# Performance work log

Hardware: AMD Instinct MI355X
Metric: run time of the kernel (lower is better)

Reference implementation:

```python
import jax, jax.numpy as jnp
import numpy as np
from jax import lax

B, C, H, W = 8, 256, 128, 128
NH = 8
HD = C // NH
EPS = 1e-5


def setup_inputs() -> dict:
    key = jax.random.key(0)
    ks = jax.random.split(key, 6)
    x = jax.random.normal(ks[0], (B, C, H, W), dtype=jnp.float32)
    dw_weight = jax.random.normal(ks[1], (C, 1, 3, 3), dtype=jnp.float32) * 0.1
    off_weight = jax.random.normal(ks[2], (NH * 2, C), dtype=jnp.float32) * 0.05
    off_bias = jnp.zeros((NH * 2,), dtype=jnp.float32)
    v_weight = jax.random.normal(ks[3], (C, C), dtype=jnp.float32) * (1.0 / np.sqrt(C))
    o_weight = jax.random.normal(ks[4], (C, C), dtype=jnp.float32) * (1.0 / np.sqrt(C))
    gamma = jnp.ones((C,), dtype=jnp.float32)
    beta = jnp.zeros((C,), dtype=jnp.float32)
    return {"x": x, "dw_weight": dw_weight, "off_weight": off_weight, "off_bias": off_bias,
            "v_weight": v_weight, "o_weight": o_weight, "gamma": gamma, "beta": beta}


def reference(x, dw_weight, off_weight, off_bias, v_weight, o_weight, gamma, beta):
    b, c, h, w = x.shape
    # --- offset branch: depthwise 3x3 + pointwise 1x1 ---
    hdw = lax.conv_general_dilated(x, dw_weight, (1, 1), 'SAME',
                                   feature_group_count=c,
                                   dimension_numbers=('NCHW', 'OIHW', 'NCHW'))
    offsets = jnp.einsum('bchw,oc->bohw', hdw, off_weight) + off_bias[None, :, None, None]
    offsets = jnp.tanh(offsets) * 0.5                      # (B, 2*NH, H, W)
    offsets = offsets.reshape(b, NH, 2, h, w)
    dy, dx = offsets[:, :, 0], offsets[:, :, 1]            # (B, NH, H, W)

    # --- value projection, split into heads ---
    V = jnp.einsum('bchw,oc->bohw', x, v_weight).reshape(b, NH, HD, h, w)

    # --- deformable bilinear sampling (grid_sample, align_corners=True, border pad) ---
    gy = jnp.linspace(-1.0, 1.0, h, dtype=x.dtype)[None, None, :, None]
    gx = jnp.linspace(-1.0, 1.0, w, dtype=x.dtype)[None, None, None, :]
    sx = jnp.clip(gx + dx, -1.0, 1.0)                      # (B, NH, H, W)
    sy = jnp.clip(gy + dy, -1.0, 1.0)
    ix = (sx + 1.0) * 0.5 * (w - 1)                        # unnormalized coords
    iy = (sy + 1.0) * 0.5 * (h - 1)
    x0f = jnp.floor(ix); y0f = jnp.floor(iy)
    wx = ix - x0f; wy = iy - y0f
    x0 = jnp.clip(x0f.astype(jnp.int32), 0, w - 1)
    x1 = jnp.clip(x0f.astype(jnp.int32) + 1, 0, w - 1)
    y0 = jnp.clip(y0f.astype(jnp.int32), 0, h - 1)
    y1 = jnp.clip(y0f.astype(jnp.int32) + 1, 0, h - 1)

    Vf = V.reshape(b, NH, HD, h * w)

    def gather(yi, xi):
        idx = (yi * w + xi).reshape(b, NH, 1, h * w)
        return jnp.take_along_axis(Vf, idx, axis=3)        # (B, NH, HD, H*W)

    wx_ = wx.reshape(b, NH, 1, h * w); wy_ = wy.reshape(b, NH, 1, h * w)
    sampled = (gather(y0, x0) * (1 - wx_) * (1 - wy_)
               + gather(y0, x1) * wx_ * (1 - wy_)
               + gather(y1, x0) * (1 - wx_) * wy_
               + gather(y1, x1) * wx_ * wy_)
    out = sampled.reshape(b, c, h, w)

    # --- output projection + GroupNorm(NH groups) + residual ---
    out = jnp.einsum('bchw,oc->bohw', out, o_weight)
    g = out.reshape(b, NH, HD * h * w)
    mu = jnp.mean(g, axis=-1, keepdims=True)
    var = jnp.mean(jnp.square(g - mu), axis=-1, keepdims=True)
    g = (g - mu) * lax.rsqrt(var + EPS)
    out = g.reshape(b, c, h, w) * gamma[None, :, None, None] + beta[None, :, None, None]
    return x + out
```

## Files before the change

### kernel.cpp

```cpp
#include <hip/hip_runtime.h>
#include <hip/hip_bf16.h>

#define B_ 8
#define C_ 256
#define H_ 128
#define W_ 128
#define HW_ 16384
#define CHW_ (C_ * HW_)
#define NH_ 8
#define HD_ 32
#define NTOT (B_ * CHW_)

typedef short short8 __attribute__((ext_vector_type(8)));
typedef float f32x4 __attribute__((ext_vector_type(4)));

__global__ __launch_bounds__(256) void wconv_kernel(const float* __restrict__ vw,
                                                    const float* __restrict__ ow,
                                                    __hip_bfloat16* __restrict__ wvb,
                                                    __hip_bfloat16* __restrict__ wob) {
    int i = blockIdx.x * 256 + threadIdx.x;
    wvb[i] = __float2bfloat16(vw[i]);
    wob[i] = __float2bfloat16(ow[i]);
}

__global__ __launch_bounds__(256) void xt_kernel(const float* __restrict__ x,
                                                 __hip_bfloat16* __restrict__ xT) {
    __shared__ float tile[64][68];
    int t = threadIdx.x;
    int p0 = blockIdx.x * 64, c0 = blockIdx.y * 64, b = blockIdx.z;
    const float* xb = x + ((size_t)b * C_ + c0) * HW_ + p0;
#pragma unroll
    for (int l = 0; l < 4; ++l) {
        int idx = t + 256 * l;
        int row = idx >> 4, cf = idx & 15;
        float4 v = *(const float4*)&xb[(size_t)row * HW_ + cf * 4];
        *(float4*)&tile[row][cf * 4] = v;
    }
    __syncthreads();
    __hip_bfloat16* op = xT + ((size_t)b * HW_ + p0) * C_ + c0;
#pragma unroll
    for (int l = 0; l < 2; ++l) {
        int idx = t + 256 * l;
        int p = idx & 63, oct = idx >> 6;
        __hip_bfloat16 arr[8];
#pragma unroll
        for (int j = 0; j < 8; ++j) arr[j] = __float2bfloat16(tile[oct * 8 + j][p]);
        *(int4*)(op + (size_t)p * C_ + oct * 8) = *(int4*)arr;
    }
}

__global__ __launch_bounds__(256) void fused_offset_kernel(const float* __restrict__ x,
                                                           const float* __restrict__ dww,
                                                           const float* __restrict__ offw,
                                                           float* __restrict__ partials) {
    __shared__ float xt[4][10][136];
    __shared__ float wT[32][16];
    __shared__ float wd[32][9];
    int t = threadIdx.x;
    int rt = blockIdx.x, cg = blockIdx.y, b = blockIdx.z;
    int h0 = rt * 8, c0 = cg * 32;
    for (int i = t; i < 512; i += 256) { int o = i >> 5, c = i & 31; wT[c][o] = offw[o * 256 + c0 + c]; }
    for (int i = t; i < 288; i += 256) { wd[i / 9][i % 9] = dww[(c0 + i / 9) * 9 + i % 9]; }
    const float* xb = x + ((size_t)b * C_ + c0) * HW_;
    int col = t & 127;
    int sb = (t >> 7) * 4;
    float acc[4][16] = {};
    for (int cc0 = 0; cc0 < 32; cc0 += 4) {
        __syncthreads();
#pragma unroll
        for (int l = 0; l < 5; ++l) {
            int idx = t + 256 * l;
            int pr = idx >> 5, c4 = idx & 31;
            int cc = pr / 10, r = pr - cc * 10;
            int gh = h0 - 1 + r;
            float4 v = make_float4(0.f, 0.f, 0.f, 0.f);
            if (gh >= 0 && gh < H_)
                v = *(const float4*)&xb[(size_t)(cc0 + cc) * HW_ + gh * W_ + c4 * 4];
            *(float4*)&xt[cc][r][4 + c4 * 4] = v;
        }
        if (t < 80) { int pr = t >> 1, side = t & 1; xt[pr / 10][pr % 10][side ? 132 : 3] = 0.f; }
        __syncthreads();
#pragma unroll
        for (int cc = 0; cc < 4; ++cc) {
            float win[6][3];
#pragma unroll
            for (int rr = 0; rr < 6; ++rr)
#pragma unroll
                for (int kk = 0; kk < 3; ++kk)
                    win[rr][kk] = xt[cc][sb + rr][col + 3 + kk];
            float w9[9];
#pragma unroll
            for (int k9 = 0; k9 < 9; ++k9) w9[k9] = wd[cc0 + cc][k9];
#pragma unroll
            for (int j = 0; j < 4; ++j) {
                float s = 0.f;
#pragma unroll
                for (int ky = 0; ky < 3; ++ky)
#pragma unroll
                    for (int kx = 0; kx < 3; ++kx)
                        s += win[j + ky][kx] * w9[ky * 3 + kx];
#pragma unroll
                for (int o = 0; o < 16; ++o) acc[j][o] += s * wT[cc0 + cc][o];
            }
        }
    }
    float* pb = partials + (size_t)(cg * 8 + b) * 16 * HW_;
#pragma unroll
    for (int o = 0; o < 16; ++o)
#pragma unroll
        for (int j = 0; j < 4; ++j)
            pb[(size_t)o * HW_ + (h0 + sb + j) * W_ + col] = acc[j][o];
}

__global__ __launch_bounds__(256) void offreduce_kernel(const float* __restrict__ partials,
                                                        const float* __restrict__ offb,
                                                        float* __restrict__ off_buf) {
    int i = blockIdx.x * 256 + threadIdx.x;
    float s = 0.f;
#pragma unroll
    for (int cg = 0; cg < 8; ++cg) s += partials[(size_t)cg * 2097152 + i];
    int o = (i >> 14) & 15;
    off_buf[i] = tanhf(s + offb[o]) * 0.5f;
}

template<bool TRANS, bool STATS>
__global__ __launch_bounds__(256) void mfma_gemm(const __hip_bfloat16* __restrict__ Wb,
                                                 const __hip_bfloat16* __restrict__ Xt,
                                                 void* __restrict__ Y,
                                                 float* __restrict__ stats) {
    __shared__ __align__(16) short Bs[128 * 256];
    int t = threadIdx.x;
    int wave = t >> 6, lane = t & 63;
    int quad = lane >> 4, l16 = lane & 15;
    int b = blockIdx.z;
    int n0 = blockIdx.x * 128, m0 = blockIdx.y * 128;
    const short* Wp = (const short*)Wb + (size_t)m0 * 256;
    const short* Xp = (const short*)Xt + ((size_t)b * HW_ + n0) * 256;

    int s = lane & 31;
    int rbase = wave * 32 + (lane >> 5);
#pragma unroll
    for (int half = 0; half < 2; ++half) {
        int4 st[8];
#pragma unroll
        for (int i = 0; i < 8; ++i) {
            int n = rbase + half * 16 + i * 2;
            st[i] = *(const int4*)(Xp + (size_t)n * 256 + s * 8);
        }
#pragma unroll
        for (int i = 0; i < 8; ++i) {
            int n = rbase + half * 16 + i * 2;
            int sw = (s & 24) | ((s ^ n) & 7);
            *(int4*)((char*)Bs + n * 512 + sw * 16) = st[i];
        }
    }

    short8 af[8][2];
#pragma unroll
    for (int ks = 0; ks < 8; ++ks)
#pragma unroll
        for (int mt = 0; mt < 2; ++mt) {
            int m = wave * 32 + mt * 16 + l16;
            af[ks][mt] = *(const short8*)(Wp + (size_t)m * 256 + ks * 32 + quad * 8);
        }

    f32x4 acc[2][8];
#pragma unroll
    for (int mt = 0; mt < 2; ++mt)
#pragma unroll
        for (int nt = 0; nt < 8; ++nt) acc[mt][nt] = (f32x4){0.f, 0.f, 0.f, 0.f};

    __syncthreads();

#pragma unroll
    for (int ks = 0; ks < 8; ++ks) {
        short8 bf[8];
#pragma unroll
        for (int nt = 0; nt < 8; ++nt) {
            int n = nt * 16 + l16;
            int slot = ks * 4 + quad;
            int sw = (slot & 24) | ((slot ^ n) & 7);
            bf[nt] = *(const short8*)((const char*)Bs + n * 512 + sw * 16);
        }
#pragma unroll
        for (int mt = 0; mt < 2; ++mt)
#pragma unroll
            for (int nt = 0; nt < 8; ++nt)
                acc[mt][nt] = __builtin_amdgcn_mfma_f32_16x16x32_bf16(af[ks][mt], bf[nt], acc[mt][nt], 0, 0, 0);
    }

    if constexpr (TRANS) {
        __hip_bfloat16* Yb = (__hip_bfloat16*)Y + (size_t)b * CHW_;
#pragma unroll
        for (int mt = 0; mt < 2; ++mt)
#pragma unroll
            for (int nt = 0; nt < 8; ++nt) {
                int m = m0 + wave * 32 + mt * 16 + quad * 4;
                int n = n0 + nt * 16 + l16;
                __hip_bfloat16 arr[4];
#pragma unroll
                for (int r = 0; r < 4; ++r) arr[r] = __float2bfloat16(acc[mt][nt][r]);
                *(int2*)((__hip_bfloat16*)Yb + (size_t)n * C_ + m) = *(int2*)arr;
            }
    } else {
        float* Yb = (float*)Y + (size_t)b * CHW_;
#pragma unroll
        for (int mt = 0; mt < 2; ++mt)
#pragma unroll
            for (int nt = 0; nt < 8; ++nt)
#pragma unroll
                for (int r = 0; r < 4; ++r) {
                    int m = m0 + wave * 32 + mt * 16 + quad * 4 + r;
                    int n = n0 + nt * 16 + l16;
                    Yb[(size_t)m * HW_ + n] = acc[mt][nt][r];
                }
    }
    if constexpr (STATS) {
        float s1 = 0.f, s2 = 0.f;
#pragma unroll
        for (int mt = 0; mt < 2; ++mt)
#pragma unroll
            for (int nt = 0; nt < 8; ++nt)
#pragma unroll
                for (int r = 0; r < 4; ++r) {
                    float v = acc[mt][nt][r];
                    s1 += v;
                    s2 += v * v;
                }
#pragma unroll
        for (int o = 32; o; o >>= 1) {
            s1 += __shfl_down(s1, o);
            s2 += __shfl_down(s2, o);
        }
        if (lane == 0) {
            int grp = b * NH_ + (m0 >> 5) + wave;
            atomicAdd(&stats[grp * 2 + 0], s1);
            atomicAdd(&stats[grp * 2 + 1], s2);
        }
    }
}

__global__ __launch_bounds__(256) void sample_kernel(const __hip_bfloat16* __restrict__ VT,
                                                     const float* __restrict__ off,
                                                     __hip_bfloat16* __restrict__ sT) {
    int t = threadIdx.x;
    int chunk = t & 3;
    int g = t >> 2;
    int head = g & 7;
    int p = blockIdx.x * 8 + (g >> 3);
    int b = blockIdx.z;
    int h = p >> 7, w = p & 127;
    const float* ob = off + ((size_t)b * 16 + head * 2) * HW_ + p;
    float dy = ob[0], dx = ob[HW_];
    float gy = h * (2.0f / 127.0f) - 1.0f;
    float gx = w * (2.0f / 127.0f) - 1.0f;
    float sx = fminf(fmaxf(gx + dx, -1.0f), 1.0f);
    float sy = fminf(fmaxf(gy + dy, -1.0f), 1.0f);
    float ix = (sx + 1.0f) * 0.5f * 127.0f;
    float iy = (sy + 1.0f) * 0.5f * 127.0f;
    float x0f = floorf(ix), y0f = floorf(iy);
    float wx = ix - x0f, wy = iy - y0f;
    int x0 = min(max((int)x0f, 0), 127);
    int x1 = min((int)x0f + 1, 127);
    int y0 = min(max((int)y0f, 0), 127);
    int y1 = min((int)y0f + 1, 127);
    float w00 = (1.f - wx) * (1.f - wy), w01 = wx * (1.f - wy);
    float w10 = (1.f - wx) * wy, w11 = wx * wy;
    const short* Vb = (const short*)VT + (size_t)b * CHW_ + head * 32 + chunk * 8;
    short8 v00 = *(const short8*)(Vb + (size_t)(y0 * W_ + x0) * C_);
    short8 v01 = *(const short8*)(Vb + (size_t)(y0 * W_ + x1) * C_);
    short8 v10 = *(const short8*)(Vb + (size_t)(y1 * W_ + x0) * C_);
    short8 v11 = *(const short8*)(Vb + (size_t)(y1 * W_ + x1) * C_);
    __hip_bfloat16 arr[8];
#pragma unroll
    for (int j = 0; j < 8; ++j) {
        float f = __bfloat162float(((const __hip_bfloat16*)&v00)[j]) * w00 +
                  __bfloat162float(((const __hip_bfloat16*)&v01)[j]) * w01 +
                  __bfloat162float(((const __hip_bfloat16*)&v10)[j]) * w10 +
                  __bfloat162float(((const __hip_bfloat16*)&v11)[j]) * w11;
        arr[j] = __float2bfloat16(f);
    }
    __hip_bfloat16* op = sT + ((size_t)b * HW_ + p) * C_ + head * 32 + chunk * 8;
    *(int4*)op = *(int4*)arr;
}

__global__ __launch_bounds__(256) void final_kernel(const float* __restrict__ x,
                                                    const float* __restrict__ stats,
                                                    const float* __restrict__ gamma,
                                                    const float* __restrict__ beta,
                                                    float* __restrict__ out) {
    int idx = (blockIdx.x * 256 + threadIdx.x) * 4;
    int c = (idx >> 14) & 255;
    int b = idx >> 22;
    int grp = b * NH_ + (c >> 5);
    const float invN = 1.0f / (float)(HD_ * HW_);
    float mu = stats[grp * 2 + 0] * invN;
    float var = stats[grp * 2 + 1] * invN - mu * mu;
    float r = rsqrtf(var + 1e-5f);
    float g = gamma[c], be = beta[c];
    float4 v = *(const float4*)&out[idx];
    float4 xv = *(const float4*)&x[idx];
    float4 o;
    o.x = xv.x + (v.x - mu) * r * g + be;
    o.y = xv.y + (v.y - mu) * r * g + be;
    o.z = xv.z + (v.z - mu) * r * g + be;
    o.w = xv.w + (v.w - mu) * r * g + be;
    *(float4*)&out[idx] = o;
}

extern "C" void kernel_launch(void* const* d_in, const int* in_sizes, int n_in,
                              void* d_out, int out_size, void* d_ws, size_t ws_size,
                              hipStream_t stream) {
    const float* x     = (const float*)d_in[0];
    const float* dww   = (const float*)d_in[1];
    const float* offw  = (const float*)d_in[2];
    const float* offb  = (const float*)d_in[3];
    const float* vw    = (const float*)d_in[4];
    const float* ow    = (const float*)d_in[5];
    const float* gamma = (const float*)d_in[6];
    const float* beta  = (const float*)d_in[7];
    float* out = (float*)d_out;
    float* ws_f = (float*)d_ws;

    float* partials = ws_f;
    float* off_buf  = ws_f + 16777216;
    float* stats    = ws_f + 18874368;
    __hip_bfloat16* wvb = (__hip_bfloat16*)(ws_f + 18874624);
    __hip_bfloat16* wob = wvb + 65536;
    __hip_bfloat16* xT  = (__hip_bfloat16*)(ws_f + 18940160);
    __hip_bfloat16* sT  = (__hip_bfloat16*)partials;
    __hip_bfloat16* vT  = (__hip_bfloat16*)out;

    wconv_kernel<<<256, 256, 0, stream>>>(vw, ow, wvb, wob);
    xt_kernel<<<dim3(256, 4, 8), 256, 0, stream>>>(x, xT);
    fused_offset_kernel<<<dim3(16, 8, 8), 256, 0, stream>>>(x, dww, offw, partials);
    offreduce_kernel<<<8192, 256, 0, stream>>>(partials, offb, off_buf);
    mfma_gemm<true, false><<<dim3(128, 2, 8), 256, 0, stream>>>(wvb, xT, (void*)vT, nullptr);
    sample_kernel<<<dim3(2048, 1, 8), 256, 0, stream>>>(vT, off_buf, sT);
    hipMemsetAsync(stats, 0, 128 * sizeof(float), stream);
    mfma_gemm<false, true><<<dim3(128, 2, 8), 256, 0, stream>>>(wob, sT, (void*)out, stats);
    final_kernel<<<NTOT / 1024, 256, 0, stream>>>(x, stats, gamma, beta, out);
}
```

Before: 566.1 us.

## Load GEMM B operand directly from global with register prefetch, drop LDS staging

The bf16 MFMA GEMM no longer stages the 128x256 activation tile in shared memory. Each wave now loads its B fragments straight from global memory through a three-deep register ring that prefetches two k-steps ahead, which removes the __syncthreads and the 64KB LDS allocation. Launch bounds ask for two blocks per SM. The cost is that all four waves read the same X tile from global/L2 (4x redundant traffic) and register pressure rises.

```diff
diff --git a/kernel.cpp b/kernel.cpp
--- a/kernel.cpp
+++ b/kernel.cpp
@@ -124,45 +124,32 @@
 }
 
 template<bool TRANS, bool STATS>
-__global__ __launch_bounds__(256) void mfma_gemm(const __hip_bfloat16* __restrict__ Wb,
-                                                 const __hip_bfloat16* __restrict__ Xt,
-                                                 void* __restrict__ Y,
-                                                 float* __restrict__ stats) {
-    __shared__ __align__(16) short Bs[128 * 256];
+__global__ __launch_bounds__(256, 2) void mfma_gemm(const __hip_bfloat16* __restrict__ Wb,
+                                                    const __hip_bfloat16* __restrict__ Xt,
+                                                    void* __restrict__ Y,
+                                                    float* __restrict__ stats) {
     int t = threadIdx.x;
     int wave = t >> 6, lane = t & 63;
     int quad = lane >> 4, l16 = lane & 15;
     int b = blockIdx.z;
     int n0 = blockIdx.x * 128, m0 = blockIdx.y * 128;
-    const short* Wp = (const short*)Wb + (size_t)m0 * 256;
+    const short* Wp = (const short*)Wb + (size_t)(m0 + wave * 32) * 256;
     const short* Xp = (const short*)Xt + ((size_t)b * HW_ + n0) * 256;
 
-    int s = lane & 31;
-    int rbase = wave * 32 + (lane >> 5);
-#pragma unroll
-    for (int half = 0; half < 2; ++half) {
-        int4 st[8];
-#pragma unroll
-        for (int i = 0; i < 8; ++i) {
-            int n = rbase + half * 16 + i * 2;
-            st[i] = *(const int4*)(Xp + (size_t)n * 256 + s * 8);
-        }
-#pragma unroll
-        for (int i = 0; i < 8; ++i) {
-            int n = rbase + half * 16 + i * 2;
-            int sw = (s & 24) | ((s ^ n) & 7);
-            *(int4*)((char*)Bs + n * 512 + sw * 16) = st[i];
-        }
-    }
-
     short8 af[8][2];
 #pragma unroll
     for (int ks = 0; ks < 8; ++ks)
 #pragma unroll
-        for (int mt = 0; mt < 2; ++mt) {
-            int m = wave * 32 + mt * 16 + l16;
-            af[ks][mt] = *(const short8*)(Wp + (size_t)m * 256 + ks * 32 + quad * 8);
-        }
+        for (int mt = 0; mt < 2; ++mt)
+            af[ks][mt] = *(const short8*)(Wp + (size_t)(mt * 16 + l16) * 256 + ks * 32 + quad * 8);
+
+    const short* Xl = Xp + (size_t)l16 * 256 + quad * 8;
+    short8 bf[3][8];
+#pragma unroll
+    for (int pf = 0; pf < 2; ++pf)
+#pragma unroll
+        for (int nt = 0; nt < 8; ++nt)
+            bf[pf][nt] = *(const short8*)(Xl + (size_t)nt * 16 * 256 + pf * 32);
 
     f32x4 acc[2][8];
 #pragma unroll
@@ -170,23 +157,18 @@
 #pragma unroll
         for (int nt = 0; nt < 8; ++nt) acc[mt][nt] = (f32x4){0.f, 0.f, 0.f, 0.f};
 
-    __syncthreads();
-
 #pragma unroll
     for (int ks = 0; ks < 8; ++ks) {
-        short8 bf[8];
-#pragma unroll
-        for (int nt = 0; nt < 8; ++nt) {
-            int n = nt * 16 + l16;
-            int slot = ks * 4 + quad;
-            int sw = (slot & 24) | ((slot ^ n) & 7);
-            bf[nt] = *(const short8*)((const char*)Bs + n * 512 + sw * 16);
-        }
-#pragma unroll
-        for (int mt = 0; mt < 2; ++mt)
+        if (ks < 6) {
 #pragma unroll
             for (int nt = 0; nt < 8; ++nt)
-                acc[mt][nt] = __builtin_amdgcn_mfma_f32_16x16x32_bf16(af[ks][mt], bf[nt], acc[mt][nt], 0, 0, 0);
+                bf[(ks + 2) % 3][nt] = *(const short8*)(Xl + (size_t)nt * 16 * 256 + (ks + 2) * 32);
+        }
+#pragma unroll
+        for (int mt = 0; mt < 2; ++mt)
+#pragma unroll
+            for (int nt = 0; nt < 8; ++nt)
+                acc[mt][nt] = __builtin_amdgcn_mfma_f32_16x16x32_bf16(af[ks][mt], bf[ks % 3][nt], acc[mt][nt], 0, 0, 0);
     }
 
     if constexpr (TRANS) {
```

Measured after the change: 641.9 us. 1.13x slower.
